# Optimization experiments

Hardware: AMD Instinct MI355X
Metric: run time of the kernel (lower is better)

## Reference

```python
import jax, jax.numpy as jnp
import numpy as np

MARGIN = 0.4
SCALE = 80.0
NEG_FILL = -1e30  # used instead of -inf for masked logsumexp (keeps grads NaN-free)

N, D, NUM_CLASSES = 8192, 128, 512


def setup_inputs() -> dict:
    key = jax.random.key(0)
    k1, k2 = jax.random.split(key)
    embeds = jax.random.normal(k1, (N, D), dtype=jnp.float32)
    labels = jax.random.randint(k2, (N,), 0, NUM_CLASSES, dtype=jnp.int64)
    return {"embeds": embeds, "labels": labels}


def _masked_lse(terms, mask):
    # stable logsumexp over axis=1 restricted to mask
    t = jnp.where(mask, terms, NEG_FILL)
    m = jnp.max(t, axis=1, keepdims=True)
    return jnp.squeeze(m, 1) + jnp.log(jnp.sum(jnp.exp(t - m), axis=1))


def reference(embeds, labels):
    # L2-normalize embeddings (F.normalize, p=2, dim=1, eps=1e-12)
    norm = jnp.maximum(jnp.linalg.norm(embeds, axis=1, keepdims=True), 1e-12)
    e = embeds / norm
    sim = e @ e.T  # [N, N]

    same = labels[:, None] == labels[None, :]
    eye = jnp.eye(labels.shape[0], dtype=bool)
    pos_mask = same & ~eye          # positives for each anchor (row)
    neg_mask = ~same                # negatives for each anchor

    # alphas are computed under no_grad in the original
    ap_alpha = jax.lax.stop_gradient(jax.nn.relu(1.0 + MARGIN - sim))
    an_alpha = jax.lax.stop_gradient(jax.nn.relu(sim + MARGIN))

    ap_term = -SCALE * ap_alpha * (sim - 1.0 + MARGIN)
    an_term = SCALE * an_alpha * (sim - MARGIN)

    np_cnt = jnp.sum(pos_mask, axis=1)  # positives per anchor
    nn_cnt = jnp.sum(neg_mask, axis=1)  # negatives per anchor
    valid = (np_cnt > 0) & (nn_cnt > 0)

    # All-triplets logsumexp factorizes: LSE over (p,n) pairs of ap_term[p]
    # equals LSE over p + log(num_neg); symmetric for an_term.
    lse_p = _masked_lse(ap_term, pos_mask)
    lse_n = _masked_lse(an_term, neg_mask)
    log_np = jnp.where(valid, jnp.log(np_cnt.astype(sim.dtype)), 0.0)
    log_nn = jnp.where(valid, jnp.log(nn_cnt.astype(sim.dtype)), 0.0)

    loss_i = jax.nn.softplus(lse_p + log_nn + lse_n + log_np)
    loss = jnp.sum(jnp.where(valid, loss_i, 0.0)) / jnp.maximum(
        jnp.sum(valid).astype(sim.dtype), 1.0)
    return loss
```

## Files before the change

### kernel.cpp

```cpp
#include <hip/hip_runtime.h>
#include <hip/hip_bf16.h>

#define NN_ 8192
#define DD_ 128
#define NSPLIT 8
#define JSPLIT (NN_ / NSPLIT)

typedef short bf16x8 __attribute__((ext_vector_type(8)));
typedef float f32x4 __attribute__((ext_vector_type(4)));

union U4 { uint4 u; bf16x8 h; };

#if __has_builtin(__builtin_amdgcn_exp2f)
#define EXP2(x) __builtin_amdgcn_exp2f(x)
#else
#define EXP2(x) __expf((x) * 0.69314718056f)
#endif

#define C1 115.415603f
#define C2 96.9491065f
#define LN2 0.69314718056f

__device__ __forceinline__ unsigned short f2bf(float f) {
    unsigned int u = __float_as_uint(f);
    unsigned int r = (u + 0x7FFFu + ((u >> 16) & 1u)) >> 16;
    return (unsigned short)r;
}


__global__ __launch_bounds__(256) void k_norm(const float* __restrict__ x,
                                              unsigned short* __restrict__ ebf) {
    int t = threadIdx.x;
    int r16 = t >> 4;
    int g = t & 15;
    int row = blockIdx.x * 16 + r16;
    const float4* xr = (const float4*)(x + (size_t)row * DD_);
    float4 v0 = xr[g * 2];
    float4 v1 = xr[g * 2 + 1];
    float ss = v0.x * v0.x + v0.y * v0.y + v0.z * v0.z + v0.w * v0.w +
               v1.x * v1.x + v1.y * v1.y + v1.z * v1.z + v1.w * v1.w;
#pragma unroll
    for (int m = 16; m < 256; m <<= 1) {
    }
#pragma unroll
    for (int m = 1; m < 16; m <<= 1) ss += __shfl_xor(ss, m);
    float inv = 1.0f / fmaxf(sqrtf(ss), 1e-12f);
    float vs[8] = {v0.x, v0.y, v0.z, v0.w, v1.x, v1.y, v1.z, v1.w};
    unsigned int p[4];
#pragma unroll
    for (int k = 0; k < 4; k++) {
        unsigned short lo = f2bf(vs[2 * k] * inv);
        unsigned short hi = f2bf(vs[2 * k + 1] * inv);
        p[k] = (unsigned int)lo | ((unsigned int)hi << 16);
    }
    uint4 out = {p[0], p[1], p[2], p[3]};
    ((uint4*)ebf)[blockIdx.x * 256 + g * 16 + r16] = out;
}

__global__ __launch_bounds__(512, 4) void k_main(const unsigned short* __restrict__ ebf,
                                                 const int* __restrict__ labels,
                                                 float* __restrict__ states) {
    const int lane = threadIdx.x & 63;
    const int wave = threadIdx.x >> 6;
    const int quad = lane >> 4;
    const int lcol = lane & 15;
    const int rowbase = blockIdx.y * 128 + wave * 16;
    const int jsplit = blockIdx.x;
    const int j0 = jsplit * JSPLIT, j1 = j0 + JSPLIT;

    const uint4* fb = (const uint4*)ebf;

    U4 afr[4];
#pragma unroll
    for (int kc = 0; kc < 4; kc++) afr[kc].u = fb[(rowbase >> 4) * 256 + kc * 64 + lane];

    int il[4];
#pragma unroll
    for (int r = 0; r < 4; r++) il[r] = labels[rowbase + quad * 4 + r];

    float S_an[4] = {0.f, 0.f, 0.f, 0.f};
    float m_p[4] = {-1e30f, -1e30f, -1e30f, -1e30f};
    float s_p[4] = {0.f, 0.f, 0.f, 0.f};
    float cnt[4] = {0.f, 0.f, 0.f, 0.f};

    U4 b0[4], b1[4];
#pragma unroll
    for (int kc = 0; kc < 4; kc++) b0[kc].u = fb[(j0 >> 4) * 256 + kc * 64 + lane];
    int jl0 = labels[j0 + lcol];
#pragma unroll
    for (int kc = 0; kc < 4; kc++) b1[kc].u = fb[((j0 + 16) >> 4) * 256 + kc * 64 + lane];
    int jl1 = labels[j0 + 16 + lcol];

    const int NIT = JSPLIT / 32;
    for (int it = 0; it < NIT; ++it) {
        const int jt = j0 + it * 32;
        const int jp = (it + 1 < NIT) ? jt + 32 : j0;

        {
            f32x4 acc = {0.f, 0.f, 0.f, 0.f};
#pragma unroll
            for (int kc = 0; kc < 4; kc++)
                acc = __builtin_amdgcn_mfma_f32_16x16x32_bf16(afr[kc].h, b0[kc].h, acc, 0, 0, 0);
            int j = jt + lcol;
#pragma unroll
            for (int r = 0; r < 4; r++) {
                float s = acc[r];
                int i = rowbase + quad * 4 + r;
                bool same = (jl0 == il[r]);
                float u = s + 0.4f;
                float a = fmaxf(u, 0.0f);
                float t2 = fmaf(a * C1, u - 0.8f, -C2);
                float e = EXP2(t2);
                S_an[r] += same ? 0.0f : e;
                cnt[r] += same ? 1.0f : 0.0f;
                if (same && j != i) {
                    float al = fmaxf(1.4f - s, 0.0f) * (-C1);
                    float tp = al * (s - 0.6f);
                    float mn = fmaxf(m_p[r], tp);
                    s_p[r] = s_p[r] * EXP2(m_p[r] - mn) + EXP2(tp - mn);
                    m_p[r] = mn;
                }
            }
        }
#pragma unroll
        for (int kc = 0; kc < 4; kc++) b0[kc].u = fb[(jp >> 4) * 256 + kc * 64 + lane];
        int jl0n = labels[jp + lcol];

        {
            f32x4 acc = {0.f, 0.f, 0.f, 0.f};
#pragma unroll
            for (int kc = 0; kc < 4; kc++)
                acc = __builtin_amdgcn_mfma_f32_16x16x32_bf16(afr[kc].h, b1[kc].h, acc, 0, 0, 0);
            int j = jt + 16 + lcol;
#pragma unroll
            for (int r = 0; r < 4; r++) {
                float s = acc[r];
                int i = rowbase + quad * 4 + r;
                bool same = (jl1 == il[r]);
                float u = s + 0.4f;
                float a = fmaxf(u, 0.0f);
                float t2 = fmaf(a * C1, u - 0.8f, -C2);
                float e = EXP2(t2);
                S_an[r] += same ? 0.0f : e;
                cnt[r] += same ? 1.0f : 0.0f;
                if (same && j != i) {
                    float al = fmaxf(1.4f - s, 0.0f) * (-C1);
                    float tp = al * (s - 0.6f);
                    float mn = fmaxf(m_p[r], tp);
                    s_p[r] = s_p[r] * EXP2(m_p[r] - mn) + EXP2(tp - mn);
                    m_p[r] = mn;
                }
            }
        }
#pragma unroll
        for (int kc = 0; kc < 4; kc++) b1[kc].u = fb[((jp + 16) >> 4) * 256 + kc * 64 + lane];
        int jl1n = labels[jp + 16 + lcol];

        jl0 = jl0n;
        jl1 = jl1n;
    }

#pragma unroll
    for (int r = 0; r < 4; r++) {
#pragma unroll
        for (int m = 1; m < 16; m <<= 1) {
            S_an[r] += __shfl_xor(S_an[r], m);
            cnt[r] += __shfl_xor(cnt[r], m);
            float m2 = __shfl_xor(m_p[r], m);
            float s2 = __shfl_xor(s_p[r], m);
            float mn = fmaxf(m_p[r], m2);
            s_p[r] = s_p[r] * EXP2(m_p[r] - mn) + s2 * EXP2(m2 - mn);
            m_p[r] = mn;
        }
    }
    if (lcol == 0) {
#pragma unroll
        for (int r = 0; r < 4; r++) {
            int i = rowbase + quad * 4 + r;
            float4 st = {m_p[r], s_p[r], S_an[r], cnt[r]};
            ((float4*)states)[(size_t)i * NSPLIT + jsplit] = st;
        }
    }
}

__global__ __launch_bounds__(256) void k_fin(const float* __restrict__ states,
                                             float* __restrict__ partials) {
    int i = blockIdx.x * 256 + threadIdx.x;
    float m_p = -1e30f, s_p = 0.f, S_an = 0.f, cnt = 0.f;
#pragma unroll
    for (int k = 0; k < NSPLIT; k++) {
        float4 st = ((const float4*)states)[(size_t)i * NSPLIT + k];
        S_an += st.z;
        cnt += st.w;
        float mn = fmaxf(m_p, st.x);
        s_p = s_p * EXP2(m_p - mn) + st.y * EXP2(st.x - mn);
        m_p = mn;
    }
    int np = (int)cnt - 1;
    int nn = NN_ - (int)cnt;
    float loss = 0.0f, v = 0.0f;
    if (np > 0 && nn > 0 && s_p > 0.f && S_an > 0.f) {
        float lse_p = LN2 * m_p + __logf(s_p);
        float lse_n = 67.2f + __logf(S_an);
        float z = lse_p + lse_n + __logf((float)np) + __logf((float)nn);
        loss = fmaxf(z, 0.0f) + log1pf(__expf(-fabsf(z)));
        v = 1.0f;
    }
#pragma unroll
    for (int m = 1; m < 64; m <<= 1) {
        loss += __shfl_xor(loss, m);
        v += __shfl_xor(v, m);
    }
    if ((threadIdx.x & 63) == 0) {
        int w = (blockIdx.x << 2) | (threadIdx.x >> 6);
        partials[w * 2] = loss;
        partials[w * 2 + 1] = v;
    }
}

__global__ void k_div(const float* __restrict__ partials, float* __restrict__ out) {
    int t = threadIdx.x;
    float loss = partials[t * 2] + partials[(t + 64) * 2];
    float v = partials[t * 2 + 1] + partials[(t + 64) * 2 + 1];
#pragma unroll
    for (int m = 1; m < 64; m <<= 1) {
        loss += __shfl_xor(loss, m);
        v += __shfl_xor(v, m);
    }
    if (t == 0) out[0] = loss / fmaxf(v, 1.0f);
}

extern "C" void kernel_launch(void* const* d_in, const int* in_sizes, int n_in,
                              void* d_out, int out_size, void* d_ws, size_t ws_size,
                              hipStream_t stream) {
    const float* embeds = (const float*)d_in[0];
    const int* labels = (const int*)d_in[1];
    float* out = (float*)d_out;

    char* ws = (char*)d_ws;
    unsigned short* ebf = (unsigned short*)ws;
    float* states = (float*)(ws + 2097152);
    float* partials = (float*)(ws + 2097152 + 1048576);

    k_norm<<<NN_ / 16, 256, 0, stream>>>(embeds, ebf);
    k_main<<<dim3(NSPLIT, NN_ / 128), 512, 0, stream>>>(ebf, labels, states);
    k_fin<<<NN_ / 256, 256, 0, stream>>>(states, partials);
    k_div<<<1, 64, 0, stream>>>(partials, out);
}
```

Baseline: 103.7 us.

## Use label histogram for counts, double column split, fuse final reduction

Computes per-class counts with an atomic histogram inside the normalize kernel, so the main loop no longer accumulates or shuffles a same-label count. It doubles the column split to launch more blocks, rewrites the exponent polynomial into a nested-FMA form, and merges the final divide kernel into k_fin with atomics and a last-block ticket. This adds a memset launch and atomic traffic, and the larger split doubles the state writes and the per-row merge work in k_fin.

```diff
diff --git a/kernel.cpp b/kernel.cpp
--- a/kernel.cpp
+++ b/kernel.cpp
@@ -3,7 +3,7 @@
 
 #define NN_ 8192
 #define DD_ 128
-#define NSPLIT 8
+#define NSPLIT 16
 #define JSPLIT (NN_ / NSPLIT)
 
 typedef short bf16x8 __attribute__((ext_vector_type(8)));
@@ -18,6 +18,7 @@
 #endif
 
 #define C1 115.415603f
+#define C1M 92.3324824f
 #define C2 96.9491065f
 #define LN2 0.69314718056f
 
@@ -29,7 +30,9 @@
 
 
 __global__ __launch_bounds__(256) void k_norm(const float* __restrict__ x,
-                                              unsigned short* __restrict__ ebf) {
+                                              const int* __restrict__ labels,
+                                              unsigned short* __restrict__ ebf,
+                                              int* __restrict__ hist) {
     int t = threadIdx.x;
     int r16 = t >> 4;
     int g = t & 15;
@@ -40,9 +43,6 @@
     float ss = v0.x * v0.x + v0.y * v0.y + v0.z * v0.z + v0.w * v0.w +
                v1.x * v1.x + v1.y * v1.y + v1.z * v1.z + v1.w * v1.w;
 #pragma unroll
-    for (int m = 16; m < 256; m <<= 1) {
-    }
-#pragma unroll
     for (int m = 1; m < 16; m <<= 1) ss += __shfl_xor(ss, m);
     float inv = 1.0f / fmaxf(sqrtf(ss), 1e-12f);
     float vs[8] = {v0.x, v0.y, v0.z, v0.w, v1.x, v1.y, v1.z, v1.w};
@@ -55,6 +55,7 @@
     }
     uint4 out = {p[0], p[1], p[2], p[3]};
     ((uint4*)ebf)[blockIdx.x * 256 + g * 16 + r16] = out;
+    if (g == 0) atomicAdd(&hist[labels[row]], 1);
 }
 
 __global__ __launch_bounds__(512, 4) void k_main(const unsigned short* __restrict__ ebf,
@@ -66,7 +67,7 @@
     const int lcol = lane & 15;
     const int rowbase = blockIdx.y * 128 + wave * 16;
     const int jsplit = blockIdx.x;
-    const int j0 = jsplit * JSPLIT, j1 = j0 + JSPLIT;
+    const int j0 = jsplit * JSPLIT;
 
     const uint4* fb = (const uint4*)ebf;
 
@@ -81,7 +82,6 @@
     float S_an[4] = {0.f, 0.f, 0.f, 0.f};
     float m_p[4] = {-1e30f, -1e30f, -1e30f, -1e30f};
     float s_p[4] = {0.f, 0.f, 0.f, 0.f};
-    float cnt[4] = {0.f, 0.f, 0.f, 0.f};
 
     U4 b0[4], b1[4];
 #pragma unroll
@@ -107,12 +107,10 @@
                 float s = acc[r];
                 int i = rowbase + quad * 4 + r;
                 bool same = (jl0 == il[r]);
-                float u = s + 0.4f;
-                float a = fmaxf(u, 0.0f);
-                float t2 = fmaf(a * C1, u - 0.8f, -C2);
+                float a = fmaxf(s + 0.4f, 0.0f);
+                float t2 = fmaf(a, fmaf(a, C1, -C1M), -C2);
                 float e = EXP2(t2);
                 S_an[r] += same ? 0.0f : e;
-                cnt[r] += same ? 1.0f : 0.0f;
                 if (same && j != i) {
                     float al = fmaxf(1.4f - s, 0.0f) * (-C1);
                     float tp = al * (s - 0.6f);
@@ -137,12 +135,10 @@
                 float s = acc[r];
                 int i = rowbase + quad * 4 + r;
                 bool same = (jl1 == il[r]);
-                float u = s + 0.4f;
-                float a = fmaxf(u, 0.0f);
-                float t2 = fmaf(a * C1, u - 0.8f, -C2);
+                float a = fmaxf(s + 0.4f, 0.0f);
+                float t2 = fmaf(a, fmaf(a, C1, -C1M), -C2);
                 float e = EXP2(t2);
                 S_an[r] += same ? 0.0f : e;
-                cnt[r] += same ? 1.0f : 0.0f;
                 if (same && j != i) {
                     float al = fmaxf(1.4f - s, 0.0f) * (-C1);
                     float tp = al * (s - 0.6f);
@@ -165,7 +161,6 @@
 #pragma unroll
         for (int m = 1; m < 16; m <<= 1) {
             S_an[r] += __shfl_xor(S_an[r], m);
-            cnt[r] += __shfl_xor(cnt[r], m);
             float m2 = __shfl_xor(m_p[r], m);
             float s2 = __shfl_xor(s_p[r], m);
             float mn = fmaxf(m_p[r], m2);
@@ -177,27 +172,31 @@
 #pragma unroll
         for (int r = 0; r < 4; r++) {
             int i = rowbase + quad * 4 + r;
-            float4 st = {m_p[r], s_p[r], S_an[r], cnt[r]};
+            float4 st = {m_p[r], s_p[r], S_an[r], 0.f};
             ((float4*)states)[(size_t)i * NSPLIT + jsplit] = st;
         }
     }
 }
 
 __global__ __launch_bounds__(256) void k_fin(const float* __restrict__ states,
-                                             float* __restrict__ partials) {
+                                             const int* __restrict__ labels,
+                                             const int* __restrict__ hist,
+                                             float* __restrict__ accum,
+                                             unsigned int* __restrict__ ticket,
+                                             float* __restrict__ out) {
     int i = blockIdx.x * 256 + threadIdx.x;
-    float m_p = -1e30f, s_p = 0.f, S_an = 0.f, cnt = 0.f;
+    int cnt = hist[labels[i]];
+    float m_p = -1e30f, s_p = 0.f, S_an = 0.f;
 #pragma unroll
     for (int k = 0; k < NSPLIT; k++) {
         float4 st = ((const float4*)states)[(size_t)i * NSPLIT + k];
         S_an += st.z;
-        cnt += st.w;
         float mn = fmaxf(m_p, st.x);
         s_p = s_p * EXP2(m_p - mn) + st.y * EXP2(st.x - mn);
         m_p = mn;
     }
-    int np = (int)cnt - 1;
-    int nn = NN_ - (int)cnt;
+    int np = cnt - 1;
+    int nn = NN_ - cnt;
     float loss = 0.0f, v = 0.0f;
     if (np > 0 && nn > 0 && s_p > 0.f && S_an > 0.f) {
         float lse_p = LN2 * m_p + __logf(s_p);
@@ -212,22 +211,19 @@
         v += __shfl_xor(v, m);
     }
     if ((threadIdx.x & 63) == 0) {
-        int w = (blockIdx.x << 2) | (threadIdx.x >> 6);
-        partials[w * 2] = loss;
-        partials[w * 2 + 1] = v;
-    }
-}
-
-__global__ void k_div(const float* __restrict__ partials, float* __restrict__ out) {
-    int t = threadIdx.x;
-    float loss = partials[t * 2] + partials[(t + 64) * 2];
-    float v = partials[t * 2 + 1] + partials[(t + 64) * 2 + 1];
-#pragma unroll
-    for (int m = 1; m < 64; m <<= 1) {
-        loss += __shfl_xor(loss, m);
-        v += __shfl_xor(v, m);
-    }
-    if (t == 0) out[0] = loss / fmaxf(v, 1.0f);
+        atomicAdd(&accum[0], loss);
+        atomicAdd(&accum[1], v);
+    }
+    __syncthreads();
+    if (threadIdx.x == 0) {
+        __threadfence();
+        unsigned int old = atomicAdd(ticket, 1u);
+        if (old == gridDim.x - 1) {
+            float L = atomicAdd(&accum[0], 0.0f);
+            float V = atomicAdd(&accum[1], 0.0f);
+            out[0] = L / fmaxf(V, 1.0f);
+        }
+    }
 }
 
 extern "C" void kernel_launch(void* const* d_in, const int* in_sizes, int n_in,
@@ -240,10 +236,13 @@
     char* ws = (char*)d_ws;
     unsigned short* ebf = (unsigned short*)ws;
     float* states = (float*)(ws + 2097152);
-    float* partials = (float*)(ws + 2097152 + 1048576);
-
-    k_norm<<<NN_ / 16, 256, 0, stream>>>(embeds, ebf);
+    int* hist = (int*)(ws + 4194304);
+    float* accum = (float*)(ws + 4194304 + 2048);
+    unsigned int* ticket = (unsigned int*)(ws + 4194304 + 2048 + 8);
+
+    hipMemsetAsync(hist, 0, 2048 + 12, stream);
+
+    k_norm<<<NN_ / 16, 256, 0, stream>>>(embeds, labels, ebf, hist);
     k_main<<<dim3(NSPLIT, NN_ / 128), 512, 0, stream>>>(ebf, labels, states);
-    k_fin<<<NN_ / 256, 256, 0, stream>>>(states, partials);
-    k_div<<<1, 64, 0, stream>>>(partials, out);
-}
+    k_fin<<<NN_ / 256, 256, 0, stream>>>(states, labels, hist, accum, ticket, out);
+}
```

Result: slower. 113.4 us (+9.4%).
